# Performance work log

Hardware: AMD Instinct MI355X
Metric: run time of the kernel (lower is better)

The kernel has to match this reference:

```python
import jax, jax.numpy as jnp
import numpy as np

AUDIO_DIM, SEM_DIM, ATTN_DIM = 512, 768, 128


def setup_inputs() -> dict:
    key = jax.random.key(0)
    ks = jax.random.split(key, 12)
    B, T, T_sem = 8, 4096, 1024
    s = lambda d: 1.0 / np.sqrt(d)
    return {
        "x_ct": jax.random.normal(ks[0], (B, AUDIO_DIM, T), jnp.float32),
        "sem_btd": jax.random.normal(ks[1], (B, T_sem, SEM_DIM), jnp.float32),
        "ln_w": jnp.ones((AUDIO_DIM,), jnp.float32),
        "ln_b": jnp.zeros((AUDIO_DIM,), jnp.float32),
        "Wq": jax.random.normal(ks[2], (AUDIO_DIM, ATTN_DIM), jnp.float32) * s(AUDIO_DIM),
        "bq": jnp.zeros((ATTN_DIM,), jnp.float32),
        "Wk": jax.random.normal(ks[3], (SEM_DIM, ATTN_DIM), jnp.float32) * s(SEM_DIM),
        "bk": jnp.zeros((ATTN_DIM,), jnp.float32),
        "Wv": jax.random.normal(ks[4], (SEM_DIM, ATTN_DIM), jnp.float32) * s(SEM_DIM),
        "bv": jnp.zeros((ATTN_DIM,), jnp.float32),
        "Wo": jax.random.normal(ks[5], (ATTN_DIM, AUDIO_DIM), jnp.float32) * s(ATTN_DIM),
        "bo": jnp.zeros((AUDIO_DIM,), jnp.float32),
    }


def _layernorm(x, w, b, eps=1e-5):
    mu = jnp.mean(x, axis=-1, keepdims=True)
    var = jnp.mean(jnp.square(x - mu), axis=-1, keepdims=True)
    return (x - mu) * jax.lax.rsqrt(var + eps) * w + b


def reference(x_ct, sem_btd, ln_w, ln_b, Wq, bq, Wk, bk, Wv, bv, Wo, bo):
    # x_ct: [B, C, T] -> [B, T, C]
    x = jnp.swapaxes(x_ct, 1, 2)
    x = _layernorm(x, ln_w, ln_b)
    Q = x @ Wq + bq                      # [B, T, A]
    K = sem_btd @ Wk + bk                # [B, S, A]
    V = sem_btd @ Wv + bv                # [B, S, A]
    scale = ATTN_DIM ** -0.5
    attn = jnp.einsum("bta,bsa->bts", Q, K) * scale
    attn = jax.nn.softmax(attn, axis=-1)  # dropout: eval mode (identity)
    ctx = jnp.einsum("bts,bsa->bta", attn, V)
    delta = ctx @ Wo + bo                # [B, T, C]
    return jnp.swapaxes(delta, 1, 2)     # [B, C, T]
```

## Files before the change

kernel.cpp:

```cpp
#include <hip/hip_runtime.h>
#include <hip/hip_bf16.h>
#include <math.h>

#define BATCH 8
#define TDIM 4096
#define SDIM 1024
#define CDIM 512
#define DDIM 768
#define ADIM 128

typedef short s8v __attribute__((ext_vector_type(8)));
typedef float f4v __attribute__((ext_vector_type(4)));

__device__ __forceinline__ short f2bf(float f) {
    unsigned u = __float_as_uint(f);
    u += 0x7fffu + ((u >> 16) & 1u);
    return (short)(u >> 16);
}
__device__ __forceinline__ float bf2f(short s) {
    return __uint_as_float(((unsigned)(unsigned short)s) << 16);
}
__device__ __forceinline__ f4v mfma16(s8v a, s8v b, f4v c) {
    return __builtin_amdgcn_mfma_f32_16x16x32_bf16(a, b, c, 0, 0, 0);
}
__device__ __forceinline__ void gl_lds16(const short* g, short* l) {
    __builtin_amdgcn_global_load_lds(
        (const __attribute__((address_space(1))) unsigned int*)g,
        (__attribute__((address_space(3))) unsigned int*)l, 16, 0, 0);
}

__global__ __launch_bounds__(256) void prep_w(
    const float* __restrict__ Wq, const float* __restrict__ Wk,
    const float* __restrict__ Wv, const float* __restrict__ Wo,
    const float* __restrict__ lnw,
    short* __restrict__ WqT, short* __restrict__ WkT,
    short* __restrict__ WvT, short* __restrict__ WoT,
    float* __restrict__ uq)
{
    int gid = blockIdx.x * 256 + threadIdx.x;
    if (blockIdx.x == 0) uq[threadIdx.x] = 0.f;
    {
        int k = gid >> 7, n = gid & 127;
        int idx = (k >> 6) * 8192 + n * 64 + ((((k >> 3) & 7) ^ (n & 7)) * 8) + (k & 7);
        WqT[idx] = f2bf(Wq[gid] * lnw[k]);
    }
    #pragma unroll
    for (int i = 0; i < 2; ++i) {
        int e = gid + i * 65536;
        if (e < 98304) {
            int k = e >> 7, n = e & 127;
            WkT[n * 768 + k] = f2bf(Wk[e]);
            WvT[n * 768 + k] = f2bf(Wv[e]);
        }
    }
    {
        int k = gid >> 9, c = gid & 511;
        WoT[c * 128 + k] = f2bf(Wo[gid]);
    }
}

__global__ __launch_bounds__(256) void prep_uv(
    const float* __restrict__ Wq, const float* __restrict__ lnw,
    const float* __restrict__ lnb,
    float* __restrict__ uq, float* __restrict__ vq)
{
    __shared__ float r1[128], r2[128];
    const int a = threadIdx.x & 127, h = threadIdx.x >> 7;
    const int c = blockIdx.x * 2 + h;
    float wv = Wq[c * 128 + a];
    float s1 = bf2f(f2bf(lnw[c] * wv));
    float s2 = lnb[c] * wv;
    if (h) { r1[a] = s1; r2[a] = s2; }
    __syncthreads();
    if (!h) {
        atomicAdd(&uq[a], s1 + r1[a]);
        atomicAdd(&vq[a], s2 + r2[a]);
    }
}

__global__ __launch_bounds__(256) void kv_proj(
    const float* __restrict__ sem,
    const short* __restrict__ WkT, const float* __restrict__ bk,
    const short* __restrict__ WvT, const float* __restrict__ bv,
    short* __restrict__ Kb, short* __restrict__ Vb)
{
    __shared__ __align__(16) short sA[32 * 40];
    __shared__ __align__(16) short sW[2][128 * 40];
    const int tid = threadIdx.x, lane = tid & 63, wave = tid >> 6;
    const int ln15 = lane & 15, q = lane >> 4, kq = q * 8;
    const int r0 = blockIdx.x * 32;
    const int b = r0 >> 10, sbase = r0 & 1023;
    const int kv = wave >> 1;
    const int mh = wave & 1;
    const int m  = mh * 16 + ln15;

    f4v acc[8];
    #pragma unroll
    for (int j = 0; j < 8; ++j) acc[j] = (f4v)0.0f;

    const int srow = tid >> 3;
    const int sk4  = (tid & 7) * 4;

    for (int kc = 0; kc < DDIM / 32; ++kc) {
        __syncthreads();
        {
            float4 f = *(const float4*)&sem[(size_t)(r0 + srow) * DDIM + kc * 32 + sk4];
            uint2 pk;
            pk.x = (unsigned short)f2bf(f.x) | ((unsigned)(unsigned short)f2bf(f.y) << 16);
            pk.y = (unsigned short)f2bf(f.z) | ((unsigned)(unsigned short)f2bf(f.w) << 16);
            *(uint2*)&sA[srow * 40 + sk4] = pk;
        }
        #pragma unroll
        for (int i = 0; i < 2; ++i) {
            int idx8 = i * 256 + tid;
            int n = idx8 >> 2, k8 = (idx8 & 3) * 8;
            *(s8v*)&sW[0][n * 40 + k8] = *(const s8v*)&WkT[(size_t)n * 768 + kc * 32 + k8];
            *(s8v*)&sW[1][n * 40 + k8] = *(const s8v*)&WvT[(size_t)n * 768 + kc * 32 + k8];
        }
        __syncthreads();
        s8v a = *(const s8v*)&sA[m * 40 + kq];
        #pragma unroll
        for (int j = 0; j < 8; ++j) {
            s8v bb = *(const s8v*)&sW[kv][(j * 16 + ln15) * 40 + kq];
            acc[j] = mfma16(a, bb, acc[j]);
        }
    }
    const int s_in_b = sbase + mh * 16 + q * 4;
    if (kv == 0) {
        #pragma unroll
        for (int j = 0; j < 8; ++j) {
            int col = j * 16 + ln15;
            float bias = bk[col];
            #pragma unroll
            for (int r = 0; r < 4; ++r)
                Kb[((size_t)b * SDIM + s_in_b + r) * ADIM + col] = f2bf(acc[j][r] + bias);
        }
    } else {
        #pragma unroll
        for (int j = 0; j < 8; ++j) {
            int col = j * 16 + ln15;
            float bias = bv[col];
            uint2 pk;
            pk.x = (unsigned short)f2bf(acc[j][0] + bias) | ((unsigned)(unsigned short)f2bf(acc[j][1] + bias) << 16);
            pk.y = (unsigned short)f2bf(acc[j][2] + bias) | ((unsigned)(unsigned short)f2bf(acc[j][3] + bias) << 16);
            *(uint2*)&Vb[((size_t)b * ADIM + col) * SDIM + s_in_b] = pk;
        }
    }
}

__global__ __launch_bounds__(512, 2) void ln_q(
    const float* __restrict__ x,
    const short* __restrict__ WqI, const float* __restrict__ uq,
    const float* __restrict__ vq, const float* __restrict__ bq,
    short* __restrict__ Qb)
{
    __shared__ __align__(16) short sX[2][128 * 72];
    __shared__ __align__(16) short sW[2][64 * 128];
    __shared__ __align__(16) float redw[8][32][4][2];
    const int tid = threadIdx.x, lane = tid & 63, wave = tid >> 6;
    const int ln15 = lane & 15, q = lane >> 4, kq = q * 8;
    const int b = blockIdx.x >> 5;
    const int t0 = (blockIdx.x & 31) * 128;
    const float* xb = x + (size_t)b * CDIM * TDIM + t0;

    const int g  = lane >> 5;
    const int L  = lane & 31;
    const int t4 = L * 4;
    const int cw = 2 * wave + g;

    float ps1[4] = {0.f,0.f,0.f,0.f}, ps2[4] = {0.f,0.f,0.f,0.f};
    const int m = wave * 16 + ln15;
    const int swzm = (m >> 2) & 7;
    f4v acc[8];
    #pragma unroll
    for (int j = 0; j < 8; ++j) acc[j] = (f4v)0.0f;

    float4 xv[4];

#define PROC_X(BUF) do {                                                      \
    _Pragma("unroll")                                                         \
    for (int i = 0; i < 4; ++i) {                                             \
        float4 v = xv[i];                                                     \
        ps1[0] += v.x; ps2[0] += v.x * v.x;                                   \
        ps1[1] += v.y; ps2[1] += v.y * v.y;                                   \
        ps1[2] += v.z; ps2[2] += v.z * v.z;                                   \
        ps1[3] += v.w; ps2[3] += v.w * v.w;                                   \
        float o0 = __shfl_xor(v.x, 32); float o1 = __shfl_xor(v.y, 32);       \
        float o2 = __shfl_xor(v.z, 32); float o3 = __shfl_xor(v.w, 32);       \
        const int cdw = i * 16 + 2 * wave;                                    \
        unsigned wA, wB; int tA, tB;                                          \
        if (g == 0) {                                                         \
            tA = t4; tB = t4 + 1;                                             \
            wA = (unsigned short)f2bf(v.x) | ((unsigned)(unsigned short)f2bf(o0) << 16); \
            wB = (unsigned short)f2bf(v.y) | ((unsigned)(unsigned short)f2bf(o1) << 16); \
        } else {                                                              \
            tA = t4 + 2; tB = t4 + 3;                                         \
            wA = (unsigned short)f2bf(o2) | ((unsigned)(unsigned short)f2bf(v.z) << 16); \
            wB = (unsigned short)f2bf(o3) | ((unsigned)(unsigned short)f2bf(v.w) << 16); \
        }                                                                     \
        *(unsigned*)&sX[BUF][tA * 72 + (((cdw >> 3) ^ ((tA >> 2) & 7)) * 8) + (cdw & 7)] = wA; \
        *(unsigned*)&sX[BUF][tB * 72 + (((cdw >> 3) ^ ((tB >> 2) & 7)) * 8) + (cdw & 7)] = wB; \
    }                                                                         \
} while (0)

    #pragma unroll
    for (int i = 0; i < 4; ++i)
        xv[i] = *(const float4*)&xb[(size_t)(i * 16 + cw) * TDIM + t4];
    #pragma unroll
    for (int i = 0; i < 2; ++i) {
        int gi = i * 512 + wave * 64;
        gl_lds16(&WqI[(size_t)(gi + lane) * 8], &sW[0][gi * 8]);
    }
    PROC_X(0);
    __syncthreads();

    for (int kc = 0; kc < 8; ++kc) {
        const int cur = kc & 1;
        if (kc < 7) {
            const float* xc = xb + (size_t)(kc + 1) * 64 * TDIM;
            #pragma unroll
            for (int i = 0; i < 4; ++i)
                xv[i] = *(const float4*)&xc[(size_t)(i * 16 + cw) * TDIM + t4];
            const short* wch = WqI + (size_t)(kc + 1) * 8192;
            #pragma unroll
            for (int i = 0; i < 2; ++i) {
                int gi = i * 512 + wave * 64;
                gl_lds16(&wch[(size_t)(gi + lane) * 8], &sW[cur ^ 1][gi * 8]);
            }
        }
        #pragma unroll
        for (int kk = 0; kk < 2; ++kk) {
            s8v a = *(const s8v*)&sX[cur][m * 72 + (((kk * 4 + q) ^ swzm) * 8)];
            #pragma unroll
            for (int j = 0; j < 8; ++j) {
                int n = j * 16 + ln15;
                s8v bb = *(const s8v*)&sW[cur][n * 64 + (((kk * 4 + q) ^ (n & 7)) * 8)];
                acc[j] = mfma16(a, bb, acc[j]);
            }
        }
        if (kc < 7) PROC_X(cur ^ 1);
        __syncthreads();
    }

    #pragma unroll
    for (int jj = 0; jj < 4; ++jj) {
        ps1[jj] += __shfl_xor(ps1[jj], 32);
        ps2[jj] += __shfl_xor(ps2[jj], 32);
    }
    if (lane < 32) {
        #pragma unroll
        for (int jj = 0; jj < 4; ++jj) {
            redw[wave][L][jj][0] = ps1[jj];
            redw[wave][L][jj][1] = ps2[jj];
        }
    }
    __syncthreads();

    float u4[8], v4[8];
    #pragma unroll
    for (int j = 0; j < 8; ++j) {
        int col = j * 16 + ln15;
        u4[j] = uq[col]; v4[j] = vq[col] + bq[col];
    }
    const float scale = 0.08838834764831845f;
    const int quad = wave * 4 + q;
    #pragma unroll
    for (int r = 0; r < 4; ++r) {
        float s1 = 0.f, s2 = 0.f;
        #pragma unroll
        for (int w = 0; w < 8; ++w) {
            float2 p = *(const float2*)&redw[w][quad][r][0];
            s1 += p.x; s2 += p.y;
        }
        float mu = s1 * (1.f / 512.f);
        float var = s2 * (1.f / 512.f) - mu * mu;
        float rs = rsqrtf(var + 1e-5f);
        int t = t0 + wave * 16 + q * 4 + r;
        #pragma unroll
        for (int j = 0; j < 8; ++j) {
            float qv = (rs * (acc[j][r] - mu * u4[j]) + v4[j]) * scale;
            Qb[((size_t)b * TDIM + t) * ADIM + (j * 16 + ln15)] = f2bf(qv);
        }
    }
#undef PROC_X
}

__global__ __launch_bounds__(256) void attn(
    const short* __restrict__ Qb, const short* __restrict__ Kb,
    const short* __restrict__ Vb, short* __restrict__ Cx)
{
    __shared__ __align__(16) short sK [2][64 * 128];
    __shared__ __align__(16) short sVT[2][128 * 64];
    __shared__ __align__(16) short sP [64 * 64];
    const int tid = threadIdx.x, lane = tid & 63, wave = tid >> 6;
    const int ln15 = lane & 15, q = lane >> 4, kq = q * 8;
    const int b = blockIdx.x >> 6;
    const int t0 = (blockIdx.x & 63) * 64;
    const int m = wave * 16 + ln15;

    const int krow = tid >> 4, kkb = tid & 15;
    const int varow = tid >> 3, vkb = tid & 7;

    s8v qf[4];
    {
        const short* qp = Qb + ((size_t)b * TDIM + t0 + m) * ADIM + kq;
        #pragma unroll
        for (int kc = 0; kc < 4; ++kc) qf[kc] = *(const s8v*)(qp + kc * 32);
    }
    s8v ones;
    #pragma unroll
    for (int j = 0; j < 8; ++j) ones[j] = (short)0x3F80;

    f4v accO[8]; f4v accL = (f4v)0.0f;
    #pragma unroll
    for (int j = 0; j < 8; ++j) accO[j] = (f4v)0.0f;

    const short* Kbase = Kb + (size_t)b * SDIM * ADIM;
    const short* Vbase = Vb + (size_t)b * ADIM * SDIM;
    s8v rk[4], rv[4];

    #pragma unroll
    for (int i = 0; i < 4; ++i) {
        rk[i] = *(const s8v*)(Kbase + (size_t)(i * 16 + krow) * ADIM + kkb * 8);
        rv[i] = *(const s8v*)(Vbase + (size_t)(i * 32 + varow) * SDIM + vkb * 8);
    }
    #pragma unroll
    for (int i = 0; i < 4; ++i) {
        int r = i * 16 + krow;
        *(s8v*)&sK[0][r * 128 + ((kkb ^ (r & 15)) * 8)] = rk[i];
        int a = i * 32 + varow;
        *(s8v*)&sVT[0][a * 64 + ((vkb ^ (a & 7)) * 8)] = rv[i];
    }
    __syncthreads();

    for (int sc = 0; sc < SDIM / 64; ++sc) {
        const int cur = sc & 1;
        if (sc < 15) {
            const int s0n = (sc + 1) * 64;
            #pragma unroll
            for (int i = 0; i < 4; ++i) {
                rk[i] = *(const s8v*)(Kbase + (size_t)(s0n + i * 16 + krow) * ADIM + kkb * 8);
                rv[i] = *(const s8v*)(Vbase + (size_t)(i * 32 + varow) * SDIM + s0n + vkb * 8);
            }
        }
        #pragma unroll
        for (int j = 0; j < 4; ++j) {
            f4v sacc = (f4v)0.0f;
            const int row = j * 16 + ln15;
            #pragma unroll
            for (int kc = 0; kc < 4; ++kc) {
                s8v bb = *(const s8v*)&sK[cur][row * 128 + (((kc * 4 + q) ^ (row & 15)) * 8)];
                sacc = mfma16(qf[kc], bb, sacc);
            }
            #pragma unroll
            for (int r = 0; r < 4; ++r) {
                float ev = __expf(sacc[r]);
                int prow = wave * 16 + q * 4 + r;
                int pcol = j * 16 + ln15;
                sP[prow * 64 + (((pcol >> 3) ^ (prow & 7)) * 8) + (pcol & 7)] = f2bf(ev);
            }
        }
        #pragma unroll
        for (int kc = 0; kc < 2; ++kc) {
            s8v pa = *(const s8v*)&sP[m * 64 + (((kc * 4 + q) ^ (m & 7)) * 8)];
            accL = mfma16(pa, ones, accL);
            #pragma unroll
            for (int j = 0; j < 8; ++j) {
                int a = j * 16 + ln15;
                s8v bb = *(const s8v*)&sVT[cur][a * 64 + (((kc * 4 + q) ^ (a & 7)) * 8)];
                accO[j] = mfma16(pa, bb, accO[j]);
            }
        }
        if (sc < 15) {
            #pragma unroll
            for (int i = 0; i < 4; ++i) {
                int r = i * 16 + krow;
                *(s8v*)&sK[cur ^ 1][r * 128 + ((kkb ^ (r & 15)) * 8)] = rk[i];
                int a = i * 32 + varow;
                *(s8v*)&sVT[cur ^ 1][a * 64 + ((vkb ^ (a & 7)) * 8)] = rv[i];
            }
        }
        __syncthreads();
    }
    #pragma unroll
    for (int r = 0; r < 4; ++r) {
        float rinv = 1.0f / accL[r];
        int t = t0 + wave * 16 + q * 4 + r;
        #pragma unroll
        for (int j = 0; j < 8; ++j) {
            int col = j * 16 + ln15;
            Cx[((size_t)b * TDIM + t) * ADIM + col] = f2bf(accO[j][r] * rinv);
        }
    }
}

__global__ __launch_bounds__(256) void out_proj(
    const short* __restrict__ Cx, const short* __restrict__ WoT,
    const float* __restrict__ bo, float* __restrict__ out)
{
    __shared__ __align__(16) short sCtx[64 * 136];
    __shared__ __align__(16) char  buf[128 * 136 * 2];
    short* sWoT = (short*)buf;
    float* outT = (float*)buf;
    const int tid = threadIdx.x, lane = tid & 63, wave = tid >> 6;
    const int ln15 = lane & 15, q = lane >> 4, kq = q * 8;
    const int b = blockIdx.x >> 8;
    const int rem = blockIdx.x & 255;
    const int t0 = (rem & 63) * 64;
    const int c0 = (rem >> 6) * 128;

    #pragma unroll
    for (int i = 0; i < 4; ++i) {
        int idx8 = i * 256 + tid;
        int row = idx8 >> 4, a8 = (idx8 & 15) * 8;
        *(s8v*)&sCtx[row * 136 + a8] = *(const s8v*)&Cx[((size_t)b * TDIM + t0 + row) * ADIM + a8];
    }
    #pragma unroll
    for (int i = 0; i < 8; ++i) {
        int idx8 = i * 256 + tid;
        int n = idx8 >> 4, k8 = (idx8 & 15) * 8;
        *(s8v*)&sWoT[n * 136 + k8] = *(const s8v*)&WoT[(size_t)(c0 + n) * ADIM + k8];
    }
    __syncthreads();
    f4v acc[8];
    #pragma unroll
    for (int j = 0; j < 8; ++j) acc[j] = (f4v)0.0f;
    const int m = wave * 16 + ln15;
    #pragma unroll
    for (int kc = 0; kc < 4; ++kc) {
        s8v a = *(const s8v*)&sCtx[m * 136 + kc * 32 + kq];
        #pragma unroll
        for (int j = 0; j < 8; ++j) {
            s8v bb = *(const s8v*)&sWoT[(j * 16 + ln15) * 136 + kc * 32 + kq];
            acc[j] = mfma16(a, bb, acc[j]);
        }
    }
    __syncthreads();
    #pragma unroll
    for (int j = 0; j < 8; ++j) {
        int cl = j * 16 + ln15;
        float bias = bo[c0 + cl];
        #pragma unroll
        for (int r = 0; r < 4; ++r) {
            int tl = wave * 16 + q * 4 + r;
            outT[cl * 68 + tl] = acc[j][r] + bias;
        }
    }
    __syncthreads();
    #pragma unroll
    for (int i = 0; i < 8; ++i) {
        int idx4 = i * 256 + tid;
        int c = idx4 >> 4, t4 = (idx4 & 15) * 4;
        float4 v = *(const float4*)&outT[c * 68 + t4];
        *(float4*)&out[((size_t)b * CDIM + c0 + c) * TDIM + t0 + t4] = v;
    }
}

extern "C" void kernel_launch(void* const* d_in, const int* in_sizes, int n_in,
                              void* d_out, int out_size, void* d_ws, size_t ws_size,
                              hipStream_t stream) {
    const float* x   = (const float*)d_in[0];
    const float* sem = (const float*)d_in[1];
    const float* lnw = (const float*)d_in[2];
    const float* lnb = (const float*)d_in[3];
    const float* Wq  = (const float*)d_in[4];
    const float* bq  = (const float*)d_in[5];
    const float* Wk  = (const float*)d_in[6];
    const float* bk  = (const float*)d_in[7];
    const float* Wv  = (const float*)d_in[8];
    const float* bv  = (const float*)d_in[9];
    const float* Wo  = (const float*)d_in[10];
    const float* bo  = (const float*)d_in[11];
    float* out = (float*)d_out;

    short* ws  = (short*)d_ws;
    short* Qb  = ws;
    short* Kb  = Qb  + (size_t)BATCH * TDIM * ADIM;
    short* Vb  = Kb  + (size_t)BATCH * SDIM * ADIM;
    short* Cx  = Vb  + (size_t)BATCH * SDIM * ADIM;
    short* WqT = Cx  + (size_t)BATCH * TDIM * ADIM;
    short* WkT = WqT + 128 * 512;
    short* WvT = WkT + 128 * 768;
    short* WoT = WvT + 128 * 768;
    float* uq  = (float*)(WoT + 512 * 128);
    float* vq  = uq + 128;

    hipLaunchKernelGGL(prep_w,  dim3(256),  dim3(256), 0, stream,
                       Wq, Wk, Wv, Wo, lnw, WqT, WkT, WvT, WoT, uq);
    hipLaunchKernelGGL(prep_uv, dim3(256),  dim3(256), 0, stream, Wq, lnw, lnb, uq, vq);
    hipLaunchKernelGGL(kv_proj, dim3(256),  dim3(256), 0, stream, sem, WkT, bk, WvT, bv, Kb, Vb);
    hipLaunchKernelGGL(ln_q,    dim3(256),  dim3(512), 0, stream, x, WqT, uq, vq, bq, Qb);
    hipLaunchKernelGGL(attn,    dim3(512),  dim3(256), 0, stream, Qb, Kb, Vb, Cx);
    hipLaunchKernelGGL(out_proj,dim3(2048), dim3(256), 0, stream, Cx, WoT, bo, out);
}
```

Before: 234.3 us.

## Split x transpose and LN stats into a separate kernel before Q projection

Adds an xpose kernel that reads x in [B,C,T] layout, transposes it in registers through shuffles and shared memory into a bf16 [B,T,C] workspace, and writes per-channel-chunk partial sums for the layernorm statistics. ln_q then loads contiguous bf16 rows with direct global-to-LDS copies instead of doing the transpose and statistics in its main loop. The aim is to shorten ln_q's critical path and give the bf16 A-operand a clean streaming load. In exchange it adds a kernel launch plus an extra write and read of a 32 MB bf16 intermediate and a partial-stats buffer.

New measurement: 247.9 us. 5.8% more time.

```diff
diff --git a/kernel.cpp b/kernel.cpp
--- a/kernel.cpp
+++ b/kernel.cpp
@@ -78,6 +78,153 @@
     }
 }
 
+__global__ __launch_bounds__(512, 2) void xpose(
+    const float* __restrict__ x, short* __restrict__ xT,
+    float* __restrict__ pstat)
+{
+    __shared__ __align__(16) short tile[2][64 * 64];
+    __shared__ float sred[2][8][64][2];
+    const int tid = threadIdx.x, lane = tid & 63, wave = tid >> 6;
+    const int c3 = lane >> 3, tg = lane & 7;
+    const int te = blockIdx.x & 7;
+    const int cc = (blockIdx.x >> 3) & 7;
+    const int b  = blockIdx.x >> 6;
+    const int c  = cc * 64 + wave * 8 + c3;
+    const float* xrow = x + ((size_t)b * CDIM + c) * TDIM + te * 512 + tg * 8;
+    short* xTb = xT + ((size_t)b * TDIM + te * 512) * CDIM + cc * 64;
+    float* pst = pstat + ((size_t)(b * 8 + cc) * TDIM + te * 512) * 2;
+
+    float4 xa = *(const float4*)(xrow);
+    float4 xb4 = *(const float4*)(xrow + 4);
+    for (int it = 0; it < 8; ++it) {
+        const int buf = it & 1;
+        float w[8] = {xa.x, xa.y, xa.z, xa.w, xb4.x, xb4.y, xb4.z, xb4.w};
+        if (it < 7) {
+            xa  = *(const float4*)(xrow + (it + 1) * 64);
+            xb4 = *(const float4*)(xrow + (it + 1) * 64 + 4);
+        }
+        #pragma unroll
+        for (int s = 0; s < 3; ++s) {
+            const int mlane = 8 << s, rb = 1 << s;
+            const bool up = (lane & mlane) != 0;
+            #pragma unroll
+            for (int i = 0; i < 8; ++i) {
+                if (i & rb) continue;
+                float lo = w[i], hi = w[i | rb];
+                float send = up ? lo : hi;
+                float got = __shfl_xor(send, mlane);
+                w[i]      = up ? got : lo;
+                w[i | rb] = up ? hi  : got;
+            }
+        }
+        const int tl = tg * 8 + c3;
+        float s1 = 0.f, s2 = 0.f;
+        #pragma unroll
+        for (int j = 0; j < 8; ++j) { s1 += w[j]; s2 += w[j] * w[j]; }
+        sred[buf][wave][tl][0] = s1;
+        sred[buf][wave][tl][1] = s2;
+        s8v pk;
+        #pragma unroll
+        for (int j = 0; j < 8; ++j) pk[j] = f2bf(w[j]);
+        *(s8v*)&tile[buf][tl * 64 + ((wave ^ c3) * 8)] = pk;
+        __syncthreads();
+        {
+            const int row = tid >> 3, part = tid & 7;
+            *(s8v*)&xTb[(size_t)(it * 64 + row) * CDIM + part * 8] =
+                *(const s8v*)&tile[buf][row * 64 + part * 8];
+        }
+        if (tid < 128) {
+            const int t_l = tid >> 1, wh = tid & 1;
+            float s = 0.f;
+            #pragma unroll
+            for (int ww = 0; ww < 8; ++ww) s += sred[buf][ww][t_l][wh];
+            pst[(it * 64 + t_l) * 2 + wh] = s;
+        }
+    }
+}
+
+__global__ __launch_bounds__(512, 2) void ln_q(
+    const short* __restrict__ xT, const short* __restrict__ WqI,
+    const float* __restrict__ pstat, const float* __restrict__ uq,
+    const float* __restrict__ vq, const float* __restrict__ bq,
+    short* __restrict__ Qb)
+{
+    __shared__ __align__(16) short sA[2][128 * 64];
+    __shared__ __align__(16) short sW[2][64 * 128];
+    __shared__ float sLN[128][2];
+    const int tid = threadIdx.x, lane = tid & 63, wave = tid >> 6;
+    const int ln15 = lane & 15, q = lane >> 4, kq = q * 8;
+    const int b = blockIdx.x >> 5;
+    const int t0 = (blockIdx.x & 31) * 128;
+    const short* xTb = xT + ((size_t)b * TDIM + t0) * CDIM;
+
+    if (tid < 256) {
+        const int t_l = tid >> 1, wh = tid & 1;
+        float s = 0.f;
+        #pragma unroll
+        for (int cc = 0; cc < 8; ++cc)
+            s += pstat[((size_t)(b * 8 + cc) * TDIM + t0 + t_l) * 2 + wh];
+        sLN[t_l][wh] = s;
+    }
+
+    const int m = wave * 16 + ln15;
+    f4v acc[8];
+    #pragma unroll
+    for (int j = 0; j < 8; ++j) acc[j] = (f4v)0.0f;
+
+#define STAGE(BUF, CC) do {                                                   \
+    _Pragma("unroll")                                                         \
+    for (int ii = 0; ii < 2; ++ii) {                                          \
+        int r0 = (wave * 2 + ii) * 8;                                         \
+        gl_lds16(&xTb[(size_t)(r0 + (lane >> 3)) * CDIM + (CC) * 64 + (lane & 7) * 8], \
+                 &sA[BUF][r0 * 64]);                                          \
+        int gi = ii * 512 + wave * 64;                                        \
+        gl_lds16(&WqI[(size_t)(CC) * 8192 + (size_t)(gi + lane) * 8],         \
+                 &sW[BUF][gi * 8]);                                           \
+    }                                                                         \
+} while (0)
+
+    STAGE(0, 0);
+    __syncthreads();
+    for (int cc = 0; cc < 8; ++cc) {
+        const int cur = cc & 1;
+        if (cc < 7) STAGE(cur ^ 1, cc + 1);
+        #pragma unroll
+        for (int kk = 0; kk < 2; ++kk) {
+            s8v a = *(const s8v*)&sA[cur][m * 64 + (((kk * 4 + q) ^ (m & 7)) * 8)];
+            #pragma unroll
+            for (int j = 0; j < 8; ++j) {
+                int n = j * 16 + ln15;
+                s8v bb = *(const s8v*)&sW[cur][n * 64 + (((kk * 4 + q) ^ (n & 7)) * 8)];
+                acc[j] = mfma16(a, bb, acc[j]);
+            }
+        }
+        __syncthreads();
+    }
+#undef STAGE
+
+    float u4[8], v4[8];
+    #pragma unroll
+    for (int j = 0; j < 8; ++j) {
+        int col = j * 16 + ln15;
+        u4[j] = uq[col]; v4[j] = vq[col] + bq[col];
+    }
+    const float scale = 0.08838834764831845f;
+    #pragma unroll
+    for (int r = 0; r < 4; ++r) {
+        const int t_l = wave * 16 + q * 4 + r;
+        float s1 = sLN[t_l][0], s2 = sLN[t_l][1];
+        float mu = s1 * (1.f / 512.f);
+        float var = s2 * (1.f / 512.f) - mu * mu;
+        float rs = rsqrtf(var + 1e-5f);
+        #pragma unroll
+        for (int j = 0; j < 8; ++j) {
+            float qv = (rs * (acc[j][r] - mu * u4[j]) + v4[j]) * scale;
+            Qb[((size_t)b * TDIM + t0 + t_l) * ADIM + (j * 16 + ln15)] = f2bf(qv);
+        }
+    }
+}
+
 __global__ __launch_bounds__(256) void kv_proj(
     const float* __restrict__ sem,
     const short* __restrict__ WkT, const float* __restrict__ bk,
@@ -146,143 +293,6 @@
             *(uint2*)&Vb[((size_t)b * ADIM + col) * SDIM + s_in_b] = pk;
         }
     }
-}
-
-__global__ __launch_bounds__(512, 2) void ln_q(
-    const float* __restrict__ x,
-    const short* __restrict__ WqI, const float* __restrict__ uq,
-    const float* __restrict__ vq, const float* __restrict__ bq,
-    short* __restrict__ Qb)
-{
-    __shared__ __align__(16) short sX[2][128 * 72];
-    __shared__ __align__(16) short sW[2][64 * 128];
-    __shared__ __align__(16) float redw[8][32][4][2];
-    const int tid = threadIdx.x, lane = tid & 63, wave = tid >> 6;
-    const int ln15 = lane & 15, q = lane >> 4, kq = q * 8;
-    const int b = blockIdx.x >> 5;
-    const int t0 = (blockIdx.x & 31) * 128;
-    const float* xb = x + (size_t)b * CDIM * TDIM + t0;
-
-    const int g  = lane >> 5;
-    const int L  = lane & 31;
-    const int t4 = L * 4;
-    const int cw = 2 * wave + g;
-
-    float ps1[4] = {0.f,0.f,0.f,0.f}, ps2[4] = {0.f,0.f,0.f,0.f};
-    const int m = wave * 16 + ln15;
-    const int swzm = (m >> 2) & 7;
-    f4v acc[8];
-    #pragma unroll
-    for (int j = 0; j < 8; ++j) acc[j] = (f4v)0.0f;
-
-    float4 xv[4];
-
-#define PROC_X(BUF) do {                                                      \
-    _Pragma("unroll")                                                         \
-    for (int i = 0; i < 4; ++i) {                                             \
-        float4 v = xv[i];                                                     \
-        ps1[0] += v.x; ps2[0] += v.x * v.x;                                   \
-        ps1[1] += v.y; ps2[1] += v.y * v.y;                                   \
-        ps1[2] += v.z; ps2[2] += v.z * v.z;                                   \
-        ps1[3] += v.w; ps2[3] += v.w * v.w;                                   \
-        float o0 = __shfl_xor(v.x, 32); float o1 = __shfl_xor(v.y, 32);       \
-        float o2 = __shfl_xor(v.z, 32); float o3 = __shfl_xor(v.w, 32);       \
-        const int cdw = i * 16 + 2 * wave;                                    \
-        unsigned wA, wB; int tA, tB;                                          \
-        if (g == 0) {                                                         \
-            tA = t4; tB = t4 + 1;                                             \
-            wA = (unsigned short)f2bf(v.x) | ((unsigned)(unsigned short)f2bf(o0) << 16); \
-            wB = (unsigned short)f2bf(v.y) | ((unsigned)(unsigned short)f2bf(o1) << 16); \
-        } else {                                                              \
-            tA = t4 + 2; tB = t4 + 3;                                         \
-            wA = (unsigned short)f2bf(o2) | ((unsigned)(unsigned short)f2bf(v.z) << 16); \
-            wB = (unsigned short)f2bf(o3) | ((unsigned)(unsigned short)f2bf(v.w) << 16); \
-        }                                                                     \
-        *(unsigned*)&sX[BUF][tA * 72 + (((cdw >> 3) ^ ((tA >> 2) & 7)) * 8) + (cdw & 7)] = wA; \
-        *(unsigned*)&sX[BUF][tB * 72 + (((cdw >> 3) ^ ((tB >> 2) & 7)) * 8) + (cdw & 7)] = wB; \
-    }                                                                         \
-} while (0)
-
-    #pragma unroll
-    for (int i = 0; i < 4; ++i)
-        xv[i] = *(const float4*)&xb[(size_t)(i * 16 + cw) * TDIM + t4];
-    #pragma unroll
-    for (int i = 0; i < 2; ++i) {
-        int gi = i * 512 + wave * 64;
-        gl_lds16(&WqI[(size_t)(gi + lane) * 8], &sW[0][gi * 8]);
-    }
-    PROC_X(0);
-    __syncthreads();
-
-    for (int kc = 0; kc < 8; ++kc) {
-        const int cur = kc & 1;
-        if (kc < 7) {
-            const float* xc = xb + (size_t)(kc + 1) * 64 * TDIM;
-            #pragma unroll
-            for (int i = 0; i < 4; ++i)
-                xv[i] = *(const float4*)&xc[(size_t)(i * 16 + cw) * TDIM + t4];
-            const short* wch = WqI + (size_t)(kc + 1) * 8192;
-            #pragma unroll
-            for (int i = 0; i < 2; ++i) {
-                int gi = i * 512 + wave * 64;
-                gl_lds16(&wch[(size_t)(gi + lane) * 8], &sW[cur ^ 1][gi * 8]);
-            }
-        }
-        #pragma unroll
-        for (int kk = 0; kk < 2; ++kk) {
-            s8v a = *(const s8v*)&sX[cur][m * 72 + (((kk * 4 + q) ^ swzm) * 8)];
-            #pragma unroll
-            for (int j = 0; j < 8; ++j) {
-                int n = j * 16 + ln15;
-                s8v bb = *(const s8v*)&sW[cur][n * 64 + (((kk * 4 + q) ^ (n & 7)) * 8)];
-                acc[j] = mfma16(a, bb, acc[j]);
-            }
-        }
-        if (kc < 7) PROC_X(cur ^ 1);
-        __syncthreads();
-    }
-
-    #pragma unroll
-    for (int jj = 0; jj < 4; ++jj) {
-        ps1[jj] += __shfl_xor(ps1[jj], 32);
-        ps2[jj] += __shfl_xor(ps2[jj], 32);
-    }
-    if (lane < 32) {
-        #pragma unroll
-        for (int jj = 0; jj < 4; ++jj) {
-            redw[wave][L][jj][0] = ps1[jj];
-            redw[wave][L][jj][1] = ps2[jj];
-        }
-    }
-    __syncthreads();
-
-    float u4[8], v4[8];
-    #pragma unroll
-    for (int j = 0; j < 8; ++j) {
-        int col = j * 16 + ln15;
-        u4[j] = uq[col]; v4[j] = vq[col] + bq[col];
-    }
-    const float scale = 0.08838834764831845f;
-    const int quad = wave * 4 + q;
-    #pragma unroll
-    for (int r = 0; r < 4; ++r) {
-        float s1 = 0.f, s2 = 0.f;
-        #pragma unroll
-        for (int w = 0; w < 8; ++w) {
-            float2 p = *(const float2*)&redw[w][quad][r][0];
-            s1 += p.x; s2 += p.y;
-        }
-        float mu = s1 * (1.f / 512.f);
-        float var = s2 * (1.f / 512.f) - mu * mu;
-        float rs = rsqrtf(var + 1e-5f);
-        int t = t0 + wave * 16 + q * 4 + r;
-        #pragma unroll
-        for (int j = 0; j < 8; ++j) {
-            float qv = (rs * (acc[j][r] - mu * u4[j]) + v4[j]) * scale;
-            Qb[((size_t)b * TDIM + t) * ADIM + (j * 16 + ln15)] = f2bf(qv);
-        }
-    }
-#undef PROC_X
 }
 
 __global__ __launch_bounds__(256) void attn(
@@ -484,12 +494,15 @@
     short* WoT = WvT + 128 * 768;
     float* uq  = (float*)(WoT + 512 * 128);
     float* vq  = uq + 128;
+    short* xTw = (short*)(vq + 128);
+    float* pst = (float*)(xTw + (size_t)BATCH * TDIM * CDIM);
 
     hipLaunchKernelGGL(prep_w,  dim3(256),  dim3(256), 0, stream,
                        Wq, Wk, Wv, Wo, lnw, WqT, WkT, WvT, WoT, uq);
     hipLaunchKernelGGL(prep_uv, dim3(256),  dim3(256), 0, stream, Wq, lnw, lnb, uq, vq);
+    hipLaunchKernelGGL(xpose,   dim3(512),  dim3(512), 0, stream, x, xTw, pst);
     hipLaunchKernelGGL(kv_proj, dim3(256),  dim3(256), 0, stream, sem, WkT, bk, WvT, bv, Kb, Vb);
-    hipLaunchKernelGGL(ln_q,    dim3(256),  dim3(512), 0, stream, x, WqT, uq, vq, bq, Qb);
+    hipLaunchKernelGGL(ln_q,    dim3(256),  dim3(512), 0, stream, xTw, WqT, pst, uq, vq, bq, Qb);
     hipLaunchKernelGGL(attn,    dim3(512),  dim3(256), 0, stream, Qb, Kb, Vb, Cx);
     hipLaunchKernelGGL(out_proj,dim3(2048), dim3(256), 0, stream, Cx, WoT, bo, out);
 }
```
